# Kernel tuning notes

Hardware: AMD Instinct MI355X
Metric: run time of the kernel (lower is better)

The kernel has to match this reference:

```python
import jax, jax.numpy as jnp
import numpy as np
from jax import lax

B, T, I, H = 64, 1024, 128, 512
DT = 0.1
EPS = 1e-8
BIG_CLAMP = 50.0
W_SCALE = 0.02  # small init so safe_exp gates stay well-behaved


def _safe_exp(v):
    return jnp.exp(jnp.minimum(v, BIG_CLAMP))


def setup_inputs() -> dict:
    key = jax.random.key(0)
    ks = jax.random.split(key, 9)
    w = lambda k, shape: jax.random.normal(k, shape, jnp.float32) * W_SCALE
    z = lambda: jnp.zeros((H,), jnp.float32)
    return {
        "x": jax.random.normal(ks[0], (B, T, I), jnp.float32),
        "Wsw": w(ks[1], (H, I)), "bsw": z(),
        "Wsm": w(ks[2], (H, I)), "bsm": z(),
        "Wss": w(ks[3], (H, I)), "bss": z(),
        "Wiw": w(ks[4], (H, H)), "biw": z(),
        "Wim": w(ks[5], (H, H)), "bim": z(),
        "Wis": w(ks[6], (H, H)), "bis": z(),
        "Wtcx": w(ks[7], (H, I)),  # time_constant weight, input slice
        "Wtch": w(ks[8], (H, H)),  # time_constant weight, hidden slice
        "btc": z(),
    }


def reference(x, Wsw, bsw, Wsm, bsm, Wss, bss,
              Wiw, biw, Wim, bim, Wis, bis, Wtcx, Wtch, btc):
    # Precompute all x-dependent projections as big GEMMs over (B,T).
    sw = jnp.einsum('bti,hi->bth', x, Wsw) + bsw
    smu = jnp.einsum('bti,hi->bth', x, Wsm) + bsm
    ssig = jnp.einsum('bti,hi->bth', x, Wss) + bss
    sensory = sw * jax.nn.sigmoid(smu) * _safe_exp(ssig)      # (B,T,H)
    tcx = jnp.einsum('bti,hi->bth', x, Wtcx) + btc            # (B,T,H)

    def step(h, inp):
        sens_t, tcx_t = inp                                   # each (B,H)
        tau = jax.nn.softplus(tcx_t + h @ Wtch.T) + 0.1
        inter = (h @ Wiw.T + biw) \
            * jax.nn.sigmoid(h @ Wim.T + bim) \
            * _safe_exp(h @ Wis.T + bis)
        dh_dt = (sens_t + inter - h) / jnp.maximum(tau, EPS)
        h_new = h + DT * dh_dt
        return h_new, h_new

    h0 = jnp.ones((B, H), x.dtype)
    xs = (jnp.swapaxes(sensory, 0, 1), jnp.swapaxes(tcx, 0, 1))  # (T,B,H)
    _, ys = lax.scan(step, h0, xs)
    return jnp.swapaxes(ys, 0, 1)  # (B,T,H)
```

## Files before the change

kernel.cpp:

```cpp
#include <hip/hip_runtime.h>
#include <math.h>

#define NB 64
#define NT 1024
#define NI 128
#define NH 512

typedef unsigned long long u64;

__global__ __launch_bounds__(256) void prep_kernel(
    const float* __restrict__ Wsw, const float* __restrict__ Wsm,
    const float* __restrict__ Wss, const float* __restrict__ Wtcx,
    float* __restrict__ WT_in, float* __restrict__ hdat,
    unsigned* __restrict__ flg)
{
  int idx = blockIdx.x * blockDim.x + threadIdx.x;
  int np  = gridDim.x * blockDim.x;
  for (int i = idx; i < NH * NI; i += np) {
    int j = i >> 7, k = i & 127;
    int o = k * 2048 + j * 4;
    WT_in[o + 0] = Wsw[i];
    WT_in[o + 1] = Wsm[i];
    WT_in[o + 2] = Wss[i];
    WT_in[o + 3] = Wtcx[i];
  }
  for (int i = idx; i < 2 * NB * NH; i += np) hdat[i] = 1.0f;
  for (int i = idx; i < 512; i += np) flg[i] = 0u;
}

__global__ __launch_bounds__(256, 2) void phase1_kernel(
    const float* __restrict__ x, const float* __restrict__ WT_in,
    const float* __restrict__ bsw, const float* __restrict__ bsm,
    const float* __restrict__ bss, const float* __restrict__ btc,
    float* __restrict__ sens, float* __restrict__ tcx)
{
  __shared__ __align__(16) float xs[32 * NI];
  const int tid = threadIdx.x;
  const int n0  = blockIdx.x * 32;

  const float4* xsrc = (const float4*)(x + (size_t)n0 * NI);
#pragma unroll
  for (int i = 0; i < 4; i++)
    ((float4*)xs)[i * 256 + tid] = xsrc[i * 256 + tid];
  __syncthreads();

  for (int jj = 0; jj < 2; jj++) {
    const int j = tid + jj * 256;
    float4 acc[32];
#pragma unroll
    for (int n = 0; n < 32; n++) acc[n] = make_float4(0.f, 0.f, 0.f, 0.f);

    const float4* wp = (const float4*)WT_in + j;
#pragma unroll 2
    for (int k = 0; k < NI; k++) {
      float4 w = wp[(size_t)k * 512];
#pragma unroll
      for (int n = 0; n < 32; n++) {
        float xv = xs[n * NI + k];
        acc[n].x = fmaf(xv, w.x, acc[n].x);
        acc[n].y = fmaf(xv, w.y, acc[n].y);
        acc[n].z = fmaf(xv, w.z, acc[n].z);
        acc[n].w = fmaf(xv, w.w, acc[n].w);
      }
    }
    const float b0 = bsw[j], b1 = bsm[j], b2v = bss[j], b3 = btc[j];
#pragma unroll 4
    for (int n = 0; n < 32; n++) {
      float sw = acc[n].x + b0;
      float sm = acc[n].y + b1;
      float ss = acc[n].z + b2v;
      float tc = acc[n].w + b3;
      float sig = 1.f / (1.f + expf(-sm));
      float se  = expf(fminf(ss, 50.f));
      size_t o = (size_t)(n0 + n) * NH + j;
      sens[o] = sw * sig * se;
      tcx[o]  = tc;
    }
  }
}

__global__ __launch_bounds__(256, 1) void phase2_kernel(
    const float* __restrict__ Wiw, const float* __restrict__ Wim,
    const float* __restrict__ Wis, const float* __restrict__ Wtch,
    const float* __restrict__ biw, const float* __restrict__ bim,
    const float* __restrict__ bis,
    const float* __restrict__ tcx, float* __restrict__ out,
    float* __restrict__ hdat, unsigned* __restrict__ flg)
{
  __shared__ __align__(16) float hl[8 * 576];
  __shared__ float red[4 * 528];

  const int tid = threadIdx.x;
  const int wv  = tid >> 6;
  const int ln  = tid & 63;
  const int bg  = blockIdx.x & 7;
  const int js  = blockIdx.x >> 3;

  const int cg = ln & 15;
  const int r  = wv * 4 + (ln >> 4);
  const int k0 = r << 5;

  const int g   = cg & 3;
  const int jl0 = cg >> 2;
  const float* Wp = (g == 0) ? Wiw : (g == 1) ? Wim : (g == 2) ? Wis : Wtch;
  float wreg[4][32];
#pragma unroll
  for (int ci = 0; ci < 4; ci++) {
    const float* wrow = Wp + (size_t)(js * 16 + jl0 + 4 * ci) * NH + k0;
#pragma unroll
    for (int kk = 0; kk < 32; kk++) wreg[ci][kk] = wrow[kk];
  }

  const int ejl = tid & 15;
  const int eb  = tid >> 4;
  const int ej  = js * 16 + ejl;
  float bw = 0.f, bm = 0.f, bs = 0.f;
  if (tid < 128) { bw = biw[ej]; bm = bim[ej]; bs = bis[ej]; }

  float* const hp0 = hdat + bg * 4096;
  float* const hp1 = hdat + NB * NH + bg * 4096;
  unsigned* const fbg0 = flg + bg * 32;
  unsigned* const fbg1 = flg + 256 + bg * 32;

  for (int t = 0; t < NT; t++) {
    const u64* dsrc = (const u64*)((t & 1) ? hp1 : hp0);
    unsigned*  ddst = (unsigned*)((t & 1) ? hp0 : hp1);
    unsigned* fsrc = (t & 1) ? fbg1 : fbg0;
    unsigned* fdst = (t & 1) ? fbg0 : fbg1;
    const unsigned want = (unsigned)t;

    float sens_v = 0.f, tcx_v = 0.f;
    size_t eidx = 0;
    if (tid < 128) {
      eidx   = ((size_t)(bg * 8 + eb) * NT + t) * NH + ej;
      sens_v = out[eidx];
      tcx_v  = tcx[eidx];
    }

    if (t > 0) {
      for (;;) {
        unsigned v = __hip_atomic_load(fsrc + (ln & 31), __ATOMIC_RELAXED,
                                       __HIP_MEMORY_SCOPE_AGENT);
        if (__all((int)(v >= want))) break;
        __builtin_amdgcn_s_sleep(1);
      }
      asm volatile("" ::: "memory");
    }

    u64 w[8];
#pragma unroll
    for (int i = 0; i < 8; i++)
      w[i] = __hip_atomic_load(dsrc + i * 256 + tid, __ATOMIC_RELAXED,
                               __HIP_MEMORY_SCOPE_AGENT);

#pragma unroll
    for (int i = 0; i < 8; i++) {
      int f  = i * 256 + tid;
      int b2 = f >> 8;
      int k  = (f & 255) << 1;
      float lo = __uint_as_float((unsigned)(w[i] & 0xFFFFFFFFull));
      float hi = __uint_as_float((unsigned)(w[i] >> 32));
      *(float2*)&hl[b2 * 576 + (k >> 5) * 36 + (k & 31)] = make_float2(lo, hi);
    }
    __syncthreads();

    float acc[4][8];
#pragma unroll
    for (int ci = 0; ci < 4; ci++)
#pragma unroll
      for (int b2 = 0; b2 < 8; b2++) acc[ci][b2] = 0.f;

    const float* hb = hl + r * 36;
#pragma unroll
    for (int b2 = 0; b2 < 8; b2++) {
#pragma unroll
      for (int kc = 0; kc < 32; kc += 4) {
        float4 hv = *(const float4*)(hb + b2 * 576 + kc);
#pragma unroll
        for (int ci = 0; ci < 4; ci++) {
          acc[ci][b2] = fmaf(wreg[ci][kc + 0], hv.x, acc[ci][b2]);
          acc[ci][b2] = fmaf(wreg[ci][kc + 1], hv.y, acc[ci][b2]);
          acc[ci][b2] = fmaf(wreg[ci][kc + 2], hv.z, acc[ci][b2]);
          acc[ci][b2] = fmaf(wreg[ci][kc + 3], hv.w, acc[ci][b2]);
        }
      }
    }

#pragma unroll
    for (int ci = 0; ci < 4; ci++)
#pragma unroll
      for (int b2 = 0; b2 < 8; b2++) {
        float v = acc[ci][b2];
        v += __shfl_xor(v, 16, 64);
        v += __shfl_xor(v, 32, 64);
        acc[ci][b2] = v;
      }
    if (ln < 16) {
#pragma unroll
      for (int ci = 0; ci < 4; ci++)
#pragma unroll
        for (int b2 = 0; b2 < 8; b2++)
          red[wv * 528 + ln * 33 + ci * 8 + b2] = acc[ci][b2];
    }
    float h_old = 0.f;
    if (tid < 128) h_old = hl[eb * 576 + (ej >> 5) * 36 + (ej & 31)];
    __syncthreads();

    if (tid < 128) {
      float vals[4];
#pragma unroll
      for (int g2 = 0; g2 < 4; g2++) {
        int c = ejl * 4 + g2;
        int o = (c & 15) * 33 + (c >> 4) * 8 + eb;
        vals[g2] = red[o] + red[528 + o] + red[1056 + o] + red[1584 + o];
      }
      float iwv = vals[0] + bw;
      float imv = vals[1] + bm;
      float isv = vals[2] + bs;
      float tch = vals[3];
      float z   = tcx_v + tch;
      float tau = fmaxf(z, 0.f) + log1pf(expf(-fabsf(z))) + 0.1f;
      float sig = 1.f / (1.f + expf(-imv));
      float inter = iwv * sig * expf(fminf(isv, 50.f));
      float dh  = (sens_v + inter - h_old) / fmaxf(tau, 1e-8f);
      float hnew = h_old + 0.1f * dh;
      __hip_atomic_store(ddst + eb * 512 + ej, __float_as_uint(hnew),
                         __ATOMIC_RELAXED, __HIP_MEMORY_SCOPE_AGENT);
      out[eidx] = hnew;
      asm volatile("s_waitcnt vmcnt(0)" ::: "memory");
    }
    __syncthreads();
    if (tid == 0)
      __hip_atomic_store(fdst + js, (unsigned)(t + 1), __ATOMIC_RELAXED,
                         __HIP_MEMORY_SCOPE_AGENT);
  }
}

extern "C" void kernel_launch(void* const* d_in, const int* in_sizes, int n_in,
                              void* d_out, int out_size, void* d_ws, size_t ws_size,
                              hipStream_t stream) {
  const float* x    = (const float*)d_in[0];
  const float* Wsw  = (const float*)d_in[1];
  const float* bsw  = (const float*)d_in[2];
  const float* Wsm  = (const float*)d_in[3];
  const float* bsm  = (const float*)d_in[4];
  const float* Wss  = (const float*)d_in[5];
  const float* bss  = (const float*)d_in[6];
  const float* Wiw  = (const float*)d_in[7];
  const float* biw  = (const float*)d_in[8];
  const float* Wim  = (const float*)d_in[9];
  const float* bim  = (const float*)d_in[10];
  const float* Wis  = (const float*)d_in[11];
  const float* bis  = (const float*)d_in[12];
  const float* Wtcx = (const float*)d_in[13];
  const float* Wtch = (const float*)d_in[14];
  const float* btc  = (const float*)d_in[15];
  float* out = (float*)d_out;

  float* ws     = (float*)d_ws;
  float* WT_in  = ws;
  float* tcx    = ws + 262144;
  float* hdat   = tcx + (size_t)NB * NT * NH;
  unsigned* flg = (unsigned*)(hdat + 2 * NB * NH);

  hipLaunchKernelGGL(prep_kernel, dim3(256), dim3(256), 0, stream,
                     Wsw, Wsm, Wss, Wtcx, WT_in, hdat, flg);

  hipLaunchKernelGGL(phase1_kernel, dim3(NB * NT / 32), dim3(256), 0, stream,
                     x, WT_in, bsw, bsm, bss, btc, out, tcx);

  hipLaunchKernelGGL(phase2_kernel, dim3(256), dim3(256), 0, stream,
                     Wiw, Wim, Wis, Wtch, biw, bim, bis,
                     tcx, out, hdat, flg);
}
```

Before: 7.862 ms.

## Split each block's batch into two interleaved halves and prefetch hidden state into LDS

Each persistent block now handles two batch groups of 4 rows instead of one group of 8, and alternates between them. While one half computes its recurrence step, the other half's hidden state is fetched straight into a padded LDS layout with global_load_lds. This is meant to hide the cross-block flag wait and global-load latency of the serial time loop behind useful compute. The hidden-state buffer is re-laid out with padding to match the LDS tile, so no register shuffle is needed. In exchange there are twice as many barriers and flag handshakes per timestep, and the dependency ordering between the two halves is more complex.

```diff
diff --git a/kernel.cpp b/kernel.cpp
--- a/kernel.cpp
+++ b/kernel.cpp
@@ -5,6 +5,9 @@
 #define NT 1024
 #define NI 128
 #define NH 512
+#define NBG 16
+#define BGSTR 3072
+#define PSTR (NBG * BGSTR)
 
 typedef unsigned long long u64;
 
@@ -24,8 +27,8 @@
     WT_in[o + 2] = Wss[i];
     WT_in[o + 3] = Wtcx[i];
   }
-  for (int i = idx; i < 2 * NB * NH; i += np) hdat[i] = 1.0f;
-  for (int i = idx; i < 512; i += np) flg[i] = 0u;
+  for (int i = idx; i < 2 * PSTR; i += np) hdat[i] = 1.0f;
+  for (int i = idx; i < 1024; i += np) flg[i] = 0u;
 }
 
 __global__ __launch_bounds__(256, 2) void phase1_kernel(
@@ -79,6 +82,107 @@
   }
 }
 
+#define DO_HALF(HLX, BGX, TX, HLY, BGY, TY)                                    \
+  {                                                                            \
+    {      \
+      const unsigned wantY = (unsigned)(TY);                                   \
+      unsigned* pf = flg + (((TY) & 1) ? 512 : 0) + (BGY) * 32;                \
+      for (;;) {                                                               \
+        unsigned v = __hip_atomic_load(pf + (ln & 31), __ATOMIC_RELAXED,       \
+                                       __HIP_MEMORY_SCOPE_AGENT);              \
+        if (__all((int)(v >= wantY))) break;                                   \
+        __builtin_amdgcn_s_sleep(1);                                           \
+      }                                                                        \
+      asm volatile("" ::: "memory");                                           \
+    }                                                                          \
+    float sens_v = 0.f, tcx_v = 0.f;                                           \
+    size_t eidx = 0;                                                           \
+    if (tid < 64) {                                                            \
+      eidx   = ((size_t)((BGX) * 4 + eb) * NT + (TX)) * NH + ej;               \
+      sens_v = out[eidx];                                                      \
+      tcx_v  = tcx[eidx];                                                      \
+    }                                                                          \
+    if ((TY) < NT) {       \
+      const float* gs = hdat + (((TY) & 1) ? PSTR : 0) + (BGY) * BGSTR;        \
+      __builtin_amdgcn_global_load_lds(                                        \
+          (const __attribute__((address_space(1))) void*)((const uint4*)gs +   \
+                                                          tid),                \
+          (__attribute__((address_space(3))) void*)((HLY) + wv * 256), 16, 0,  \
+          16);                                                                 \
+      __builtin_amdgcn_global_load_lds(                                        \
+          (const __attribute__((address_space(1))) void*)((const uint4*)gs +   \
+                                                          256 + tid),          \
+          (__attribute__((address_space(3))) void*)((HLY) + 1024 + wv * 256),  \
+          16, 0, 16);                                                          \
+      __builtin_amdgcn_global_load_lds(                                        \
+          (const __attribute__((address_space(1))) void*)((const uint4*)gs +   \
+                                                          512 + tid),          \
+          (__attribute__((address_space(3))) void*)((HLY) + 2048 + wv * 256),  \
+          16, 0, 16);                                                          \
+    }                                                                          \
+    __syncthreads();                   \
+    float acc[4][4];                                                           \
+    _Pragma("unroll") for (int ci = 0; ci < 4; ci++)                           \
+        _Pragma("unroll") for (int b2 = 0; b2 < 4; b2++) acc[ci][b2] = 0.f;    \
+    {                                                                          \
+      const float* hb0 = (HLX) + r * 168;                                      \
+      _Pragma("unroll") for (int b2 = 0; b2 < 4; b2++) {                       \
+        _Pragma("unroll") for (int c = 0; c < 8; c++) {                        \
+          float4 hv = *(const float4*)(hb0 + b2 * 36 + c * 4);                 \
+          _Pragma("unroll") for (int ci = 0; ci < 4; ci++) {                   \
+            acc[ci][b2] = fmaf(wreg[ci][c * 4 + 0], hv.x, acc[ci][b2]);        \
+            acc[ci][b2] = fmaf(wreg[ci][c * 4 + 1], hv.y, acc[ci][b2]);        \
+            acc[ci][b2] = fmaf(wreg[ci][c * 4 + 2], hv.z, acc[ci][b2]);        \
+            acc[ci][b2] = fmaf(wreg[ci][c * 4 + 3], hv.w, acc[ci][b2]);        \
+          }                                                                    \
+        }                                                                      \
+      }                                                                        \
+    }                                                                          \
+    _Pragma("unroll") for (int ci = 0; ci < 4; ci++)                           \
+        _Pragma("unroll") for (int b2 = 0; b2 < 4; b2++) {                     \
+      float v = acc[ci][b2];                                                   \
+      v += __shfl_xor(v, 16, 64);                                              \
+      v += __shfl_xor(v, 32, 64);                                              \
+      acc[ci][b2] = v;                                                         \
+    }                                                                          \
+    if (ln < 16) {                                                             \
+      _Pragma("unroll") for (int ci = 0; ci < 4; ci++)                         \
+          _Pragma("unroll") for (int b2 = 0; b2 < 4; b2++)                     \
+              red[wv * 272 + ln * 17 + ci * 4 + b2] = acc[ci][b2];             \
+    }                                                                          \
+    float h_old = 0.f;                                                         \
+    if (tid < 64) h_old = (HLX)[eoff];                                         \
+    __syncthreads();                                      \
+    if (tid < 64) {                                                            \
+      float vals[4];                                                           \
+      _Pragma("unroll") for (int g2 = 0; g2 < 4; g2++) {                       \
+        int c = ejl * 4 + g2;                                                  \
+        int o = (c & 15) * 17 + (c >> 4) * 4 + eb;                             \
+        vals[g2] = red[o] + red[272 + o] + red[544 + o] + red[816 + o];        \
+      }                                                                        \
+      float iwv = vals[0] + bw;                                                \
+      float imv = vals[1] + bm;                                                \
+      float isv = vals[2] + bs;                                                \
+      float z   = tcx_v + vals[3];                                             \
+      float tau = fmaxf(z, 0.f) + log1pf(expf(-fabsf(z))) + 0.1f;              \
+      float sig = 1.f / (1.f + expf(-imv));                                    \
+      float inter = iwv * sig * expf(fminf(isv, 50.f));                        \
+      float dh  = (sens_v + inter - h_old) / fmaxf(tau, 1e-8f);                \
+      float hnew = h_old + 0.1f * dh;                                          \
+      unsigned* dd = (unsigned*)(hdat + ((((TX) + 1) & 1) ? PSTR : 0) +        \
+                                 (BGX) * BGSTR);                               \
+      __hip_atomic_store(dd + eoff, __float_as_uint(hnew), __ATOMIC_RELAXED,   \
+                         __HIP_MEMORY_SCOPE_AGENT);                            \
+      out[eidx] = hnew;                                                        \
+      asm volatile("s_waitcnt vmcnt(0)" ::: "memory");                         \
+    }                                                                          \
+    __syncthreads();                     \
+    if (tid == 0)                                                              \
+      __hip_atomic_store(flg + ((((TX) + 1) & 1) ? 512 : 0) + (BGX) * 32 + js, \
+                         (unsigned)((TX) + 1), __ATOMIC_RELAXED,               \
+                         __HIP_MEMORY_SCOPE_AGENT);                            \
+  }
+
 __global__ __launch_bounds__(256, 1) void phase2_kernel(
     const float* __restrict__ Wiw, const float* __restrict__ Wim,
     const float* __restrict__ Wis, const float* __restrict__ Wtch,
@@ -87,14 +191,17 @@
     const float* __restrict__ tcx, float* __restrict__ out,
     float* __restrict__ hdat, unsigned* __restrict__ flg)
 {
-  __shared__ __align__(16) float hl[8 * 576];
-  __shared__ float red[4 * 528];
+  __shared__ __align__(16) float hlA[3072];
+  __shared__ __align__(16) float hlB[3072];
+  __shared__ float red[4 * 272];
 
   const int tid = threadIdx.x;
   const int wv  = tid >> 6;
   const int ln  = tid & 63;
-  const int bg  = blockIdx.x & 7;
+  const int pc  = blockIdx.x & 7;
   const int js  = blockIdx.x >> 3;
+  const int bgA = pc;
+  const int bgB = pc + 8;
 
   const int cg = ln & 15;
   const int r  = wv * 4 + (ln >> 4);
@@ -114,125 +221,30 @@
   const int ejl = tid & 15;
   const int eb  = tid >> 4;
   const int ej  = js * 16 + ejl;
+  const int eoff = ((ej >> 5) * 168) + eb * 36 + (ej & 31);
   float bw = 0.f, bm = 0.f, bs = 0.f;
-  if (tid < 128) { bw = biw[ej]; bm = bim[ej]; bs = bis[ej]; }
-
-  float* const hp0 = hdat + bg * 4096;
-  float* const hp1 = hdat + NB * NH + bg * 4096;
-  unsigned* const fbg0 = flg + bg * 32;
-  unsigned* const fbg1 = flg + 256 + bg * 32;
+  if (tid < 64) { bw = biw[ej]; bm = bim[ej]; bs = bis[ej]; }
+
+  {
+    const float* gs = hdat + bgA * BGSTR;
+    __builtin_amdgcn_global_load_lds(
+        (const __attribute__((address_space(1))) void*)((const uint4*)gs + tid),
+        (__attribute__((address_space(3))) void*)(hlA + wv * 256), 16, 0, 16);
+    __builtin_amdgcn_global_load_lds(
+        (const __attribute__((address_space(1))) void*)((const uint4*)gs + 256 +
+                                                        tid),
+        (__attribute__((address_space(3))) void*)(hlA + 1024 + wv * 256), 16, 0,
+        16);
+    __builtin_amdgcn_global_load_lds(
+        (const __attribute__((address_space(1))) void*)((const uint4*)gs + 512 +
+                                                        tid),
+        (__attribute__((address_space(3))) void*)(hlA + 2048 + wv * 256), 16, 0,
+        16);
+  }
 
   for (int t = 0; t < NT; t++) {
-    const u64* dsrc = (const u64*)((t & 1) ? hp1 : hp0);
-    unsigned*  ddst = (unsigned*)((t & 1) ? hp0 : hp1);
-    unsigned* fsrc = (t & 1) ? fbg1 : fbg0;
-    unsigned* fdst = (t & 1) ? fbg0 : fbg1;
-    const unsigned want = (unsigned)t;
-
-    float sens_v = 0.f, tcx_v = 0.f;
-    size_t eidx = 0;
-    if (tid < 128) {
-      eidx   = ((size_t)(bg * 8 + eb) * NT + t) * NH + ej;
-      sens_v = out[eidx];
-      tcx_v  = tcx[eidx];
-    }
-
-    if (t > 0) {
-      for (;;) {
-        unsigned v = __hip_atomic_load(fsrc + (ln & 31), __ATOMIC_RELAXED,
-                                       __HIP_MEMORY_SCOPE_AGENT);
-        if (__all((int)(v >= want))) break;
-        __builtin_amdgcn_s_sleep(1);
-      }
-      asm volatile("" ::: "memory");
-    }
-
-    u64 w[8];
-#pragma unroll
-    for (int i = 0; i < 8; i++)
-      w[i] = __hip_atomic_load(dsrc + i * 256 + tid, __ATOMIC_RELAXED,
-                               __HIP_MEMORY_SCOPE_AGENT);
-
-#pragma unroll
-    for (int i = 0; i < 8; i++) {
-      int f  = i * 256 + tid;
-      int b2 = f >> 8;
-      int k  = (f & 255) << 1;
-      float lo = __uint_as_float((unsigned)(w[i] & 0xFFFFFFFFull));
-      float hi = __uint_as_float((unsigned)(w[i] >> 32));
-      *(float2*)&hl[b2 * 576 + (k >> 5) * 36 + (k & 31)] = make_float2(lo, hi);
-    }
-    __syncthreads();
-
-    float acc[4][8];
-#pragma unroll
-    for (int ci = 0; ci < 4; ci++)
-#pragma unroll
-      for (int b2 = 0; b2 < 8; b2++) acc[ci][b2] = 0.f;
-
-    const float* hb = hl + r * 36;
-#pragma unroll
-    for (int b2 = 0; b2 < 8; b2++) {
-#pragma unroll
-      for (int kc = 0; kc < 32; kc += 4) {
-        float4 hv = *(const float4*)(hb + b2 * 576 + kc);
-#pragma unroll
-        for (int ci = 0; ci < 4; ci++) {
-          acc[ci][b2] = fmaf(wreg[ci][kc + 0], hv.x, acc[ci][b2]);
-          acc[ci][b2] = fmaf(wreg[ci][kc + 1], hv.y, acc[ci][b2]);
-          acc[ci][b2] = fmaf(wreg[ci][kc + 2], hv.z, acc[ci][b2]);
-          acc[ci][b2] = fmaf(wreg[ci][kc + 3], hv.w, acc[ci][b2]);
-        }
-      }
-    }
-
-#pragma unroll
-    for (int ci = 0; ci < 4; ci++)
-#pragma unroll
-      for (int b2 = 0; b2 < 8; b2++) {
-        float v = acc[ci][b2];
-        v += __shfl_xor(v, 16, 64);
-        v += __shfl_xor(v, 32, 64);
-        acc[ci][b2] = v;
-      }
-    if (ln < 16) {
-#pragma unroll
-      for (int ci = 0; ci < 4; ci++)
-#pragma unroll
-        for (int b2 = 0; b2 < 8; b2++)
-          red[wv * 528 + ln * 33 + ci * 8 + b2] = acc[ci][b2];
-    }
-    float h_old = 0.f;
-    if (tid < 128) h_old = hl[eb * 576 + (ej >> 5) * 36 + (ej & 31)];
-    __syncthreads();
-
-    if (tid < 128) {
-      float vals[4];
-#pragma unroll
-      for (int g2 = 0; g2 < 4; g2++) {
-        int c = ejl * 4 + g2;
-        int o = (c & 15) * 33 + (c >> 4) * 8 + eb;
-        vals[g2] = red[o] + red[528 + o] + red[1056 + o] + red[1584 + o];
-      }
-      float iwv = vals[0] + bw;
-      float imv = vals[1] + bm;
-      float isv = vals[2] + bs;
-      float tch = vals[3];
-      float z   = tcx_v + tch;
-      float tau = fmaxf(z, 0.f) + log1pf(expf(-fabsf(z))) + 0.1f;
-      float sig = 1.f / (1.f + expf(-imv));
-      float inter = iwv * sig * expf(fminf(isv, 50.f));
-      float dh  = (sens_v + inter - h_old) / fmaxf(tau, 1e-8f);
-      float hnew = h_old + 0.1f * dh;
-      __hip_atomic_store(ddst + eb * 512 + ej, __float_as_uint(hnew),
-                         __ATOMIC_RELAXED, __HIP_MEMORY_SCOPE_AGENT);
-      out[eidx] = hnew;
-      asm volatile("s_waitcnt vmcnt(0)" ::: "memory");
-    }
-    __syncthreads();
-    if (tid == 0)
-      __hip_atomic_store(fdst + js, (unsigned)(t + 1), __ATOMIC_RELAXED,
-                         __HIP_MEMORY_SCOPE_AGENT);
+    DO_HALF(hlA, bgA, t, hlB, bgB, t);
+    DO_HALF(hlB, bgB, t, hlA, bgA, t + 1);
   }
 }
 
@@ -261,7 +273,7 @@
   float* WT_in  = ws;
   float* tcx    = ws + 262144;
   float* hdat   = tcx + (size_t)NB * NT * NH;
-  unsigned* flg = (unsigned*)(hdat + 2 * NB * NH);
+  unsigned* flg = (unsigned*)(hdat + 2 * PSTR);
 
   hipLaunchKernelGGL(prep_kernel, dim3(256), dim3(256), 0, stream,
                      Wsw, Wsm, Wss, Wtcx, WT_in, hdat, flg);
```

Result: slower. 10.20 ms (+29.8%).
